# Kernel optimization log

Measured on AMD Instinct MI355X. Metric: run time of the kernel, lower is better.

## Reference

```python
import jax, jax.numpy as jnp
import numpy as np

N = 100000       # node_num / batch_node_num
E = 1_600_000    # edges (avg degree 16)
IN_DIM = 256
OUT_DIM = 128
SLOPE = 0.1


def setup_inputs() -> dict:
    key = jax.random.key(0)
    k0, k1, k2, k3, k4 = jax.random.split(key, 5)
    node_feats = jax.random.normal(k0, (N, IN_DIM), jnp.float32)
    W = jax.random.normal(k1, (OUT_DIM, IN_DIM), jnp.float32) * (1.0 / np.sqrt(IN_DIM))
    b = jnp.zeros((OUT_DIM,), jnp.float32)
    # a ~ kaiming_normal for shape [2*out_dim, 1]; stored flat here
    a = jax.random.normal(k2, (2 * OUT_DIM,), jnp.float32) * np.sqrt(2.0 / (2 * OUT_DIM))
    src = jax.random.randint(k3, (E,), 0, N, dtype=jnp.int32)
    dst = jax.random.randint(k4, (E,), 0, N, dtype=jnp.int32)
    return {"node_feats": node_feats, "W": W, "b": b, "a": a, "src": src, "dst": dst}


def reference(node_feats, W, b, a, src, dst):
    n = node_feats.shape[0]
    d = W.shape[0]
    # out_linear_layer
    emb = node_feats @ W.T + b                      # [N, D]
    # append self-loop edges (original_node_edge)
    loop = jnp.arange(n, dtype=src.dtype)
    s = jnp.concatenate([src, loop])                # [E+N]
    t = jnp.concatenate([dst, loop])                # [E+N]
    # concat(emb[s], emb[t]) @ a  ==  emb[s] @ a[:D] + emb[t] @ a[D:]
    logits = emb[s] @ a[:d] + emb[t] @ a[d:]        # [E+N]
    score = jnp.exp(jax.nn.leaky_relu(logits, negative_slope=SLOPE))
    # sparse.mm(matrix, emb) and sparse.mm(matrix, ones): segment sums over src rows
    num = jax.ops.segment_sum(score[:, None] * emb[t], s, num_segments=n)  # [N, D]
    den = jax.ops.segment_sum(score, s, num_segments=n)                    # [N]
    return num / den[:, None]
```

## Files before the change

### kernel.cpp

```cpp
#include <hip/hip_runtime.h>
#include <hip/hip_bf16.h>

#define IN_DIM 256
#define OUT_DIM 128
#define SLOPE 0.1f

typedef __attribute__((ext_vector_type(8))) _Float16 f16x8;
typedef __attribute__((ext_vector_type(4))) float f32x4;
typedef __attribute__((ext_vector_type(8))) unsigned short u16x8;

__global__ void convert_w_kernel(const float* __restrict__ W,
                                 _Float16* __restrict__ Wf, int total) {
  int i = blockIdx.x * blockDim.x + threadIdx.x;
  if (i < total) Wf[i] = (_Float16)W[i];
}

__global__ __launch_bounds__(256) void gemm_mfma_kernel(
    const float* __restrict__ A,
    const _Float16* __restrict__ Wf,
    const float* __restrict__ bias,
    const float* __restrict__ avec,
    float* __restrict__ emb,
    float* __restrict__ a1,
    float* __restrict__ a2,
    int N) {
  __shared__ _Float16 wlds[32768];

  const int tid = threadIdx.x;

#pragma unroll
  for (int i = 0; i < 16; ++i) {
    int chunk = tid + i * 256;
    int f = chunk << 4;
    int n = f >> 9;
    int o = f & 511;
    int osrc = o ^ ((n & 7) << 4);
    u16x8 v = *(const u16x8*)((const char*)Wf + (size_t)n * 512 + osrc);
    *(u16x8*)((char*)wlds + f) = v;
  }
  __syncthreads();

  const int lane = tid & 63;
  const int wave = tid >> 6;
  const int m0 = blockIdx.x * 64 + wave * 16;
  const int lr = lane & 15;
  const int kg = lane >> 4;

  int arow = m0 + lr;
  if (arow > N - 1) arow = N - 1;
  const float* aptr = A + (size_t)arow * IN_DIM + kg * 8;

  f32x4 acc[8];
#pragma unroll
  for (int t = 0; t < 8; ++t) acc[t] = (f32x4)(0.f);

  const int rowbase = lr * 512;
  const int swzmask = (lr & 7) << 4;

  for (int k0 = 0; k0 < IN_DIM; k0 += 32) {
    float4 q0 = *(const float4*)(aptr + k0);
    float4 q1 = *(const float4*)(aptr + k0 + 4);
    float qs[8] = {q0.x, q0.y, q0.z, q0.w, q1.x, q1.y, q1.z, q1.w};
    f16x8 ahi, alo;
#pragma unroll
    for (int j = 0; j < 8; ++j) {
      float x = qs[j];
      _Float16 h = (_Float16)x;
      ahi[j] = h;
      alo[j] = (_Float16)(x - (float)h);
    }
    const int ko = ((k0 * 2 + kg * 16) ^ swzmask);
    const char* wl = (const char*)wlds + rowbase + ko;
#pragma unroll
    for (int t = 0; t < 8; ++t) {
      f16x8 bf = *(const f16x8*)(wl + t * 8192);
      acc[t] = __builtin_amdgcn_mfma_f32_16x16x32_f16(ahi, bf, acc[t], 0, 0, 0);
      acc[t] = __builtin_amdgcn_mfma_f32_16x16x32_f16(alo, bf, acc[t], 0, 0, 0);
    }
  }

  float p1[4] = {0.f, 0.f, 0.f, 0.f};
  float p2[4] = {0.f, 0.f, 0.f, 0.f};
#pragma unroll
  for (int t = 0; t < 8; ++t) {
    const int c = t * 16 + lr;
    const float bv = bias[c];
    const float av1 = avec[c];
    const float av2 = avec[OUT_DIM + c];
#pragma unroll
    for (int v = 0; v < 4; ++v) {
      const int r = m0 + kg * 4 + v;
      const float e = acc[t][v] + bv;
      if (r < N) emb[(size_t)r * OUT_DIM + c] = e;
      p1[v] += e * av1;
      p2[v] += e * av2;
    }
  }
#pragma unroll
  for (int v = 0; v < 4; ++v) {
#pragma unroll
    for (int d = 1; d < 16; d <<= 1) {
      p1[v] += __shfl_xor(p1[v], d, 64);
      p2[v] += __shfl_xor(p2[v], d, 64);
    }
  }
  if (lr == 0) {
#pragma unroll
    for (int v = 0; v < 4; ++v) {
      const int r = m0 + kg * 4 + v;
      if (r < N) { a1[r] = p1[v]; a2[r] = p2[v]; }
    }
  }
}

__global__ void hist_kernel(const int* __restrict__ src, int* __restrict__ deg,
                            int E) {
  int i = blockIdx.x * blockDim.x + threadIdx.x;
  if (i < E) atomicAdd(&deg[src[i]], 1);
}

__global__ __launch_bounds__(1024) void scan1_kernel(
    const int* __restrict__ deg, int* __restrict__ offset,
    int* __restrict__ blocksum, int N) {
  __shared__ int tmp[16];
  const int tid = threadIdx.x;
  const int lane = tid & 63;
  const int wave = tid >> 6;
  int i = blockIdx.x * 1024 + tid;
  int v = (i < N) ? deg[i] : 0;
  int x = v;
#pragma unroll
  for (int d = 1; d < 64; d <<= 1) {
    int y = __shfl_up(x, d, 64);
    if (lane >= d) x += y;
  }
  if (lane == 63) tmp[wave] = x;
  __syncthreads();
  if (tid < 16) {
    int wv = tmp[tid];
#pragma unroll
    for (int d = 1; d < 16; d <<= 1) {
      int y = __shfl_up(wv, d, 16);
      if (tid >= d) wv += y;
    }
    tmp[tid] = wv;
  }
  __syncthreads();
  int waveoff = (wave == 0) ? 0 : tmp[wave - 1];
  if (i < N) offset[i] = waveoff + x - v;
  if (tid == 0) blocksum[blockIdx.x] = tmp[15];
}

__global__ __launch_bounds__(1024) void scan2_kernel(int* __restrict__ blocksum,
                                                     int nb) {
  __shared__ int tmp[16];
  const int tid = threadIdx.x;
  const int lane = tid & 63;
  const int wave = tid >> 6;
  int v = (tid < nb) ? blocksum[tid] : 0;
  int x = v;
#pragma unroll
  for (int d = 1; d < 64; d <<= 1) {
    int y = __shfl_up(x, d, 64);
    if (lane >= d) x += y;
  }
  if (lane == 63) tmp[wave] = x;
  __syncthreads();
  if (tid < 16) {
    int wv = tmp[tid];
#pragma unroll
    for (int d = 1; d < 16; d <<= 1) {
      int y = __shfl_up(wv, d, 16);
      if (tid >= d) wv += y;
    }
    tmp[tid] = wv;
  }
  __syncthreads();
  int waveoff = (wave == 0) ? 0 : tmp[wave - 1];
  if (tid < nb) blocksum[tid] = waveoff + x - v;
}

__global__ void scan3_kernel(int* __restrict__ offset,
                             const int* __restrict__ blocksum,
                             int* __restrict__ pos, int N) {
  int i = blockIdx.x * blockDim.x + threadIdx.x;
  if (i < N) {
    int o = offset[i] + blocksum[i >> 10];
    offset[i] = o;
    pos[i] = o;
  }
}

__global__ void scatter_kernel(const int* __restrict__ src,
                               const int* __restrict__ dst,
                               int* __restrict__ pos,
                               int* __restrict__ tsorted, int E) {
  int i = blockIdx.x * blockDim.x + threadIdx.x;
  if (i < E) {
    int p = atomicAdd(&pos[src[i]], 1);
    tsorted[p] = dst[i];
  }
}

__global__ __launch_bounds__(256) void aggregate_kernel(
    const float* __restrict__ emb, const float* __restrict__ a1,
    const float* __restrict__ a2, const int* __restrict__ offset,
    const int* __restrict__ deg, const int* __restrict__ tsorted,
    float* __restrict__ out, int N) {
  int n = (int)((blockIdx.x * (size_t)blockDim.x + threadIdx.x) >> 6);
  int lane = threadIdx.x & 63;
  if (n >= N) return;
  const int q = lane >> 4;
  const int sub = lane & 15;

  const float as = a1[n];
  const int beg = offset[n];
  const int cnt = deg[n];
  const int items = cnt + 1;
  const int niter = (items + 3) >> 2;

  float4 acc0 = make_float4(0.f, 0.f, 0.f, 0.f);
  float4 acc1 = make_float4(0.f, 0.f, 0.f, 0.f);
  float den = 0.f;

  int idx = q;
  int t = (idx == 0 || idx > cnt) ? n : tsorted[beg + idx - 1];
  float at = a2[t];

  for (int i = 0; i < niter; ++i) {
    const bool valid = (idx < items);
    const float* row = emb + (size_t)t * OUT_DIM + sub * 8;
    const float4 v0 = *(const float4*)row;
    const float4 v1 = *(const float4*)(row + 4);
    const float logit = as + at;
    const int idxn = idx + 4;
    if (i + 1 < niter) {
      int tn = (idxn <= cnt) ? tsorted[beg + idxn - 1] : n;
      t = tn;
      at = a2[tn];
    }
    idx = idxn;
    const float sc = valid ? __expf(logit > 0.f ? logit : SLOPE * logit) : 0.f;
    acc0.x += sc * v0.x; acc0.y += sc * v0.y;
    acc0.z += sc * v0.z; acc0.w += sc * v0.w;
    acc1.x += sc * v1.x; acc1.y += sc * v1.y;
    acc1.z += sc * v1.z; acc1.w += sc * v1.w;
    den += sc;
  }

#pragma unroll
  for (int d = 16; d < 64; d <<= 1) {
    acc0.x += __shfl_xor(acc0.x, d, 64);
    acc0.y += __shfl_xor(acc0.y, d, 64);
    acc0.z += __shfl_xor(acc0.z, d, 64);
    acc0.w += __shfl_xor(acc0.w, d, 64);
    acc1.x += __shfl_xor(acc1.x, d, 64);
    acc1.y += __shfl_xor(acc1.y, d, 64);
    acc1.z += __shfl_xor(acc1.z, d, 64);
    acc1.w += __shfl_xor(acc1.w, d, 64);
    den    += __shfl_xor(den,    d, 64);
  }

  if (q == 0) {
    const float inv = 1.0f / den;
    float* op = out + (size_t)n * OUT_DIM + sub * 8;
    *(float4*)op = make_float4(acc0.x * inv, acc0.y * inv, acc0.z * inv,
                               acc0.w * inv);
    *(float4*)(op + 4) = make_float4(acc1.x * inv, acc1.y * inv, acc1.z * inv,
                                     acc1.w * inv);
  }
}

extern "C" void kernel_launch(void* const* d_in, const int* in_sizes, int n_in,
                              void* d_out, int out_size, void* d_ws,
                              size_t ws_size, hipStream_t stream) {
  const float* node_feats = (const float*)d_in[0];
  const float* W = (const float*)d_in[1];
  const float* bias = (const float*)d_in[2];
  const float* avec = (const float*)d_in[3];
  const int* src = (const int*)d_in[4];
  const int* dst = (const int*)d_in[5];
  float* out = (float*)d_out;

  const int OUT = in_sizes[2];
  const int IN = in_sizes[1] / OUT;
  const int N = in_sizes[0] / IN;
  const int E = in_sizes[4];
  const int NB = (N + 1023) / 1024;
  const int WTOT = in_sizes[1];

  char* p = (char*)d_ws;
  auto alloc = [&](size_t bytes) {
    void* r = (void*)p;
    p += (bytes + 255) & ~(size_t)255;
    return r;
  };
  float* emb = (float*)alloc((size_t)N * OUT * sizeof(float));
  float* a1 = (float*)alloc((size_t)N * sizeof(float));
  float* a2 = (float*)alloc((size_t)N * sizeof(float));
  int* deg = (int*)alloc((size_t)N * sizeof(int));
  int* offset = (int*)alloc((size_t)N * sizeof(int));
  int* pos = (int*)alloc((size_t)N * sizeof(int));
  int* blocksum = (int*)alloc((size_t)NB * sizeof(int));
  int* tsorted = (int*)alloc((size_t)E * sizeof(int));
  _Float16* Wfp = (_Float16*)alloc((size_t)WTOT * sizeof(_Float16));

  hipMemsetAsync(deg, 0, (size_t)N * sizeof(int), stream);

  convert_w_kernel<<<(WTOT + 255) / 256, 256, 0, stream>>>(W, Wfp, WTOT);
  hist_kernel<<<(E + 255) / 256, 256, 0, stream>>>(src, deg, E);

  gemm_mfma_kernel<<<(N + 63) / 64, 256, 0, stream>>>(
      node_feats, Wfp, bias, avec, emb, a1, a2, N);

  scan1_kernel<<<NB, 1024, 0, stream>>>(deg, offset, blocksum, N);
  scan2_kernel<<<1, 1024, 0, stream>>>(blocksum, NB);
  scan3_kernel<<<(N + 255) / 256, 256, 0, stream>>>(offset, blocksum, pos, N);

  scatter_kernel<<<(E + 255) / 256, 256, 0, stream>>>(src, dst, pos, tsorted,
                                                      E);

  aggregate_kernel<<<(N + 3) / 4, 256, 0, stream>>>(emb, a1, a2, offset, deg,
                                                    tsorted, out, N);
}
```

Measured before the change: 515.8 us.

## Replace per-node atomic scatter with two-pass bucketed counting sort

The CSR build no longer scatters each edge straight to its per-node slot with a global atomic. Edges are first scattered into 128-node buckets using per-bucket atomic cursors, and each bucket is then sorted locally with shared-memory atomics. The goal is more local, coherent writes for the edge list and cheaper atomics in the second pass. The cost is two extra kernels, extra temporary arrays (ed, es) and a second pass over the edges. The global atomics now contend on far fewer addresses, which could serialise them.

```diff
diff --git a/kernel.cpp b/kernel.cpp
--- a/kernel.cpp
+++ b/kernel.cpp
@@ -181,24 +181,58 @@
 }
 
 __global__ void scan3_kernel(int* __restrict__ offset,
-                             const int* __restrict__ blocksum,
-                             int* __restrict__ pos, int N) {
+                             const int* __restrict__ blocksum, int N) {
   int i = blockIdx.x * blockDim.x + threadIdx.x;
-  if (i < N) {
-    int o = offset[i] + blocksum[i >> 10];
-    offset[i] = o;
-    pos[i] = o;
-  }
-}
-
-__global__ void scatter_kernel(const int* __restrict__ src,
-                               const int* __restrict__ dst,
-                               int* __restrict__ pos,
-                               int* __restrict__ tsorted, int E) {
+  if (i < N) offset[i] += blocksum[i >> 10];
+}
+
+__global__ void cursor_init_kernel(const int* __restrict__ offset,
+                                   int* __restrict__ cursor, int NBK) {
+  int b = blockIdx.x * blockDim.x + threadIdx.x;
+  if (b < NBK) cursor[b] = offset[b << 7];
+}
+
+__global__ void bucket_scatter_kernel(const int* __restrict__ src,
+                                      const int* __restrict__ dst,
+                                      int* __restrict__ cursor,
+                                      int* __restrict__ ed,
+                                      unsigned char* __restrict__ es, int E) {
   int i = blockIdx.x * blockDim.x + threadIdx.x;
   if (i < E) {
-    int p = atomicAdd(&pos[src[i]], 1);
-    tsorted[p] = dst[i];
+    int s = src[i];
+    int p = atomicAdd(&cursor[s >> 7], 1);
+    ed[p] = dst[i];
+    es[p] = (unsigned char)(s & 127);
+  }
+}
+
+__global__ __launch_bounds__(256) void bucket_sort_kernel(
+    const int* __restrict__ ed, const unsigned char* __restrict__ es,
+    const int* __restrict__ offset, int* __restrict__ tsorted, int N, int E) {
+  __shared__ int lcnt[128];
+  __shared__ int lcur[128];
+  const int tid = threadIdx.x;
+  const int n0 = blockIdx.x << 7;
+  const int base = offset[n0];
+  const int bend = (n0 + 128 < N) ? offset[n0 + 128] : E;
+
+  if (tid < 128) lcnt[tid] = 0;
+  __syncthreads();
+  for (int i = base + tid; i < bend; i += 256)
+    atomicAdd(&lcnt[es[i]], 1);
+  __syncthreads();
+  if (tid == 0) {
+    int run = base;
+#pragma unroll 8
+    for (int j = 0; j < 128; ++j) {
+      lcur[j] = run;
+      run += lcnt[j];
+    }
+  }
+  __syncthreads();
+  for (int i = base + tid; i < bend; i += 256) {
+    int p = atomicAdd(&lcur[es[i]], 1);
+    tsorted[p] = ed[i];
   }
 }
 
@@ -287,6 +321,7 @@
   const int N = in_sizes[0] / IN;
   const int E = in_sizes[4];
   const int NB = (N + 1023) / 1024;
+  const int NBK = (N + 127) / 128;
   const int WTOT = in_sizes[1];
 
   char* p = (char*)d_ws;
@@ -300,9 +335,11 @@
   float* a2 = (float*)alloc((size_t)N * sizeof(float));
   int* deg = (int*)alloc((size_t)N * sizeof(int));
   int* offset = (int*)alloc((size_t)N * sizeof(int));
-  int* pos = (int*)alloc((size_t)N * sizeof(int));
   int* blocksum = (int*)alloc((size_t)NB * sizeof(int));
+  int* cursor = (int*)alloc((size_t)NBK * sizeof(int));
   int* tsorted = (int*)alloc((size_t)E * sizeof(int));
+  int* ed = (int*)alloc((size_t)E * sizeof(int));
+  unsigned char* es = (unsigned char*)alloc((size_t)E);
   _Float16* Wfp = (_Float16*)alloc((size_t)WTOT * sizeof(_Float16));
 
   hipMemsetAsync(deg, 0, (size_t)N * sizeof(int), stream);
@@ -315,10 +352,13 @@
 
   scan1_kernel<<<NB, 1024, 0, stream>>>(deg, offset, blocksum, N);
   scan2_kernel<<<1, 1024, 0, stream>>>(blocksum, NB);
-  scan3_kernel<<<(N + 255) / 256, 256, 0, stream>>>(offset, blocksum, pos, N);
-
-  scatter_kernel<<<(E + 255) / 256, 256, 0, stream>>>(src, dst, pos, tsorted,
-                                                      E);
+  scan3_kernel<<<(N + 255) / 256, 256, 0, stream>>>(offset, blocksum, N);
+  cursor_init_kernel<<<(NBK + 255) / 256, 256, 0, stream>>>(offset, cursor,
+                                                            NBK);
+
+  bucket_scatter_kernel<<<(E + 255) / 256, 256, 0, stream>>>(src, dst, cursor,
+                                                             ed, es, E);
+  bucket_sort_kernel<<<NBK, 256, 0, stream>>>(ed, es, offset, tsorted, N, E);
 
   aggregate_kernel<<<(N + 3) / 4, 256, 0, stream>>>(emb, a1, a2, offset, deg,
                                                     tsorted, out, N);
```

New measurement: 784.2 us. 1.52x slower.
